# Optimization experiments

Hardware: AMD Instinct MI355X
Metric: run time of the kernel (lower is better)

Reference implementation:

```python
import jax, jax.numpy as jnp
import numpy as np

NEG_BIG = -9e15
ALPHA = 0.2  # leaky relu slope


def setup_inputs() -> dict:
    key = jax.random.key(0)
    k_h, k_adj, k_W, k_a = jax.random.split(key, 4)
    N, F_in, F_out = 8192, 512, 64
    h = jax.random.normal(k_h, (N, F_in), dtype=jnp.float32)
    adj = jax.random.randint(k_adj, (N, N), 0, 2, dtype=jnp.int32)
    adj = adj.at[jnp.arange(N), jnp.arange(N)].set(1)  # self-loops (add_self_loops)
    # xavier_uniform with gain=1.414
    limW = 1.414 * np.sqrt(6.0 / (F_in + F_out))
    W = jax.random.uniform(k_W, (F_in, F_out), jnp.float32, -limW, limW)
    lima = 1.414 * np.sqrt(6.0 / (2 * F_out + 1))
    a = jax.random.uniform(k_a, (2 * F_out, 1), jnp.float32, -lima, lima)
    return {"h": h, "adj": adj, "W": W, "a": a}


def reference(h, adj, W, a):
    F_out = W.shape[1]
    Wh = h @ W                                  # [N, F_out]
    # a_input[i,j] = concat(Wh[i], Wh[j]); a_input @ a == Wh@a1 + (Wh@a2)^T
    a1, a2 = a[:F_out, 0], a[F_out:, 0]
    src = Wh @ a1                               # [N]
    dst = Wh @ a2                               # [N]
    e = jax.nn.leaky_relu(src[:, None] + dst[None, :], ALPHA)  # [N, N]
    att = jnp.where(adj > 0, e, NEG_BIG)
    att = jax.nn.softmax(att, axis=1)
    # dropout is identity in eval mode (training=False)
    return att @ Wh                             # [N, F_out]
```

## Files before the change

kernel.cpp:

```cpp
#include <hip/hip_runtime.h>
#include <hip/hip_bf16.h>

#define N 8192
#define FIN 512
#define FOUT 64
#define L2E 1.44269504089f
#define SPLIT 8
#define MSTRIDE 34

typedef __attribute__((address_space(1))) const void* gas_cptr;
typedef __attribute__((address_space(3))) void* las_ptr;
typedef float f32x4 __attribute__((ext_vector_type(4)));
typedef short bf16x8 __attribute__((ext_vector_type(8)));

#if __has_builtin(__builtin_amdgcn_exp2f)
#define EXP2(x) __builtin_amdgcn_exp2f(x)
#else
#define EXP2(x) exp2f(x)
#endif

static __device__ __forceinline__ unsigned short f2bf_rne(float f) {
  unsigned u = __float_as_uint(f);
  u += 0x7FFFu + ((u >> 16) & 1u);
  return (unsigned short)(u >> 16);
}
static __device__ __forceinline__ unsigned fkey(float f) {
  unsigned u = __float_as_uint(f);
  return (u & 0x80000000u) ? ~u : (u | 0x80000000u);
}

__global__ __launch_bounds__(256) void k_wh(
    const float* __restrict__ h, const float* __restrict__ W,
    const float* __restrict__ a, unsigned short* __restrict__ WhT,
    float* __restrict__ src2, float* __restrict__ dst2,
    unsigned* __restrict__ dmaxk) {
  __shared__ __attribute__((aligned(16))) char wts[64 * 512 * 2];
  __shared__ __attribute__((aligned(16))) char hsb[2][64 * 64 * 2];

  const int t = threadIdx.x;
  const int w = t >> 6;
  const int ll = t & 63;
  const int lc = ll & 15;
  const int row0 = blockIdx.x * 64;

  {
    const int k0 = t * 2;
#pragma unroll
    for (int f4 = 0; f4 < 16; ++f4) {
      float4 x0 = *reinterpret_cast<const float4*>(&W[(size_t)k0 * FOUT + f4 * 4]);
      float4 x1 = *reinterpret_cast<const float4*>(&W[(size_t)(k0 + 1) * FOUT + f4 * 4]);
      const float e0[4] = {x0.x, x0.y, x0.z, x0.w};
      const float e1[4] = {x1.x, x1.y, x1.z, x1.w};
#pragma unroll
      for (int e = 0; e < 4; ++e) {
        int f = f4 * 4 + e;
        int bb = f * 1024 + k0 * 2;
        bb ^= (f & 7) << 4;
        *reinterpret_cast<ushort2*>(wts + bb) =
            make_ushort2(f2bf_rne(e0[e]), f2bf_rne(e1[e]));
      }
    }
  }
  __syncthreads();

  f32x4 acc[4];
#pragma unroll
  for (int c = 0; c < 4; ++c) acc[c] = (f32x4){0.f, 0.f, 0.f, 0.f};

  const int hrow = 16 * w + (ll >> 2);
  const float* hbase = &h[(size_t)(row0 + hrow) * FIN + (ll & 3) * 16];

#define LOADH(dst, kc)                                                        \
  do {                                                                        \
    dst[0] = *reinterpret_cast<const float4*>(hbase + (kc));                  \
    dst[1] = *reinterpret_cast<const float4*>(hbase + (kc) + 4);              \
    dst[2] = *reinterpret_cast<const float4*>(hbase + (kc) + 8);              \
    dst[3] = *reinterpret_cast<const float4*>(hbase + (kc) + 12);             \
  } while (0)

#define WRITEH(buf, src)                                                      \
  do {                                                                        \
    int bb0 = hrow * 128 + (ll & 3) * 32;                                     \
    bb0 ^= (hrow & 7) << 4;                                                   \
    _Pragma("unroll") for (int q = 0; q < 4; ++q) {                           \
      ushort4 u = make_ushort4(f2bf_rne(src[q].x), f2bf_rne(src[q].y),        \
                               f2bf_rne(src[q].z), f2bf_rne(src[q].w));       \
      *reinterpret_cast<ushort4*>(hsb[buf] + (bb0 ^ (q * 8))) = u;            \
    }                                                                         \
  } while (0)

#define MFMA_CHUNK(buf, kcb)                                                  \
  do {                                                                        \
    _Pragma("unroll") for (int k0 = 0; k0 < 2; ++k0) {                        \
      int arow = 16 * w + lc;                                                 \
      int ab = arow * 128 + k0 * 64 + ((ll >> 4) << 4);                       \
      ab ^= (arow & 7) << 4;                                                  \
      bf16x8 af = *reinterpret_cast<const bf16x8*>(hsb[buf] + ab);            \
      _Pragma("unroll") for (int c = 0; c < 4; ++c) {                         \
        int f = c * 16 + lc;                                                  \
        int bb = f * 1024 + (kcb) + k0 * 64 + ((ll >> 4) << 4);               \
        bb ^= (f & 7) << 4;                                                   \
        bf16x8 bfr = *reinterpret_cast<const bf16x8*>(wts + bb);              \
        acc[c] = __builtin_amdgcn_mfma_f32_16x16x32_bf16(af, bfr, acc[c], 0, 0, 0); \
      }                                                                       \
    }                                                                         \
  } while (0)

  float4 ha[4], hb[4];
  LOADH(ha, 0);
#pragma unroll
  for (int c2 = 0; c2 < 4; ++c2) {
    WRITEH(0, ha);
    LOADH(hb, (2 * c2 + 1) * 64);
    MFMA_CHUNK(0, (2 * c2) * 128);
    WRITEH(1, hb);
    if (c2 < 3) LOADH(ha, (2 * c2 + 2) * 64);
    MFMA_CHUNK(1, (2 * c2 + 1) * 128);
  }

  float a1v[4], a2v[4];
#pragma unroll
  for (int c = 0; c < 4; ++c) {
    a1v[c] = a[c * 16 + lc];
    a2v[c] = a[FOUT + c * 16 + lc];
  }
  float p1[4], p2[4];
#pragma unroll
  for (int q = 0; q < 4; ++q) {
    p1[q] = acc[0][q] * a1v[0] + acc[1][q] * a1v[1] + acc[2][q] * a1v[2] + acc[3][q] * a1v[3];
    p2[q] = acc[0][q] * a2v[0] + acc[1][q] * a2v[1] + acc[2][q] * a2v[2] + acc[3][q] * a2v[3];
  }
#pragma unroll
  for (int msk = 8; msk >= 1; msk >>= 1)
#pragma unroll
    for (int q = 0; q < 4; ++q) {
      p1[q] += __shfl_xor(p1[q], msk);
      p2[q] += __shfl_xor(p2[q], msk);
    }
#pragma unroll
  for (int q = 0; q < 4; ++q) { p1[q] *= L2E; p2[q] *= L2E; }

  const int r0 = row0 + 16 * w + ((ll >> 4) << 2);
  if (lc == 0) {
#pragma unroll
    for (int q = 0; q < 4; ++q) { src2[r0 + q] = p1[q]; dst2[r0 + q] = p2[q]; }
  }
#pragma unroll
  for (int c = 0; c < 4; ++c) {
    ushort4 u = make_ushort4(f2bf_rne(acc[c][0]), f2bf_rne(acc[c][1]),
                             f2bf_rne(acc[c][2]), f2bf_rne(acc[c][3]));
    *reinterpret_cast<ushort4*>(&WhT[(size_t)(c * 16 + lc) * N + r0]) = u;
  }
  float wm = fmaxf(fmaxf(p2[0], p2[1]), fmaxf(p2[2], p2[3]));
  wm = fmaxf(wm, __shfl_xor(wm, 16));
  wm = fmaxf(wm, __shfl_xor(wm, 32));
  if (ll == 0) atomicMax(dmaxk, fkey(wm));
#undef LOADH
#undef WRITEH
#undef MFMA_CHUNK
}

__global__ __launch_bounds__(256) void k_attn(
    const int* __restrict__ adj, const unsigned short* __restrict__ WhT,
    const float* __restrict__ src2, const float* __restrict__ dst2,
    const unsigned* __restrict__ dmaxk, float* __restrict__ out,
    float* __restrict__ Opart, float* __restrict__ lpart, const int split) {
  __shared__ unsigned mskd[64 * MSTRIDE];
  __shared__ __attribute__((aligned(16))) char pbs[8192];

  const int t = threadIdx.x;
  const int w = t >> 6;
  const int ll = t & 63;
  const int rg = t >> 4;
  const int cg = t & 15;
  const int i0 = rg * 4;
  const int lc = ll & 15;
  const int g16 = (ll >> 4) << 4;
  const int g8 = (ll >> 4) << 3;
  const int row0 = blockIdx.x * 64;
  const int jlen = N / split;
  const int jbase = blockIdx.y * jlen;

  unsigned kk = dmaxk[0];
  const float dmax2 = (kk & 0x80000000u) ? __uint_as_float(kk & 0x7FFFFFFFu)
                                         : __uint_as_float(~kk);

  float s2v[4], m2[4], l[4];
#pragma unroll
  for (int r = 0; r < 4; ++r) {
    s2v[r] = src2[row0 + i0 + r];
    float x = s2v[r] + dmax2;
    m2[r] = fmaxf(x, 0.2f * x);
    l[r] = 0.f;
  }

  f32x4 acc[4];
#pragma unroll
  for (int c = 0; c < 4; ++c) acc[c] = (f32x4){0.f, 0.f, 0.f, 0.f};

  const int bsh = (cg & 7) * 4;

  for (int mt = 0; mt < jlen; mt += 1024) {
    const int mbase = jbase + mt;

#pragma unroll 1
    for (int s = 0; s < 16; ++s) {
      const int row = 16 * w + s;
      const int* ar = adj + (size_t)(row0 + row) * N + mbase;
      unsigned x[16];
#pragma unroll
      for (int k = 0; k < 16; ++k) x[k] = ar[k * 64 + ll];
      unsigned long long b[16];
#pragma unroll
      for (int k = 0; k < 16; ++k) b[k] = __ballot(x[k] != 0);
      if (ll == 0) {
        unsigned long long* mrow =
            reinterpret_cast<unsigned long long*>(&mskd[row * MSTRIDE]);
#pragma unroll
        for (int k = 0; k < 16; ++k) mrow[k] = b[k];
      }
    }
    __syncthreads();

    unsigned mw[4], nmw[4];
    float dv[4], ndv[4];
#pragma unroll
    for (int r = 0; r < 4; ++r)
      mw[r] = mskd[(i0 + r) * MSTRIDE + (cg >> 3)];
    {
      float4 d_ = *reinterpret_cast<const float4*>(&dst2[mbase + cg * 4]);
      dv[0] = d_.x; dv[1] = d_.y; dv[2] = d_.z; dv[3] = d_.w;
    }

#pragma unroll 1
    for (int jt2 = 0; jt2 < 16; ++jt2) {
      const int j0 = mbase + jt2 * 64;

      bf16x8 bfr[2][4];
#pragma unroll
      for (int k0 = 0; k0 < 2; ++k0)
#pragma unroll
        for (int c = 0; c < 4; ++c)
          bfr[k0][c] = *reinterpret_cast<const bf16x8*>(
              &WhT[(size_t)(c * 16 + lc) * N + j0 + k0 * 32 + g8]);

      if (jt2 + 1 < 16) {
#pragma unroll
        for (int r = 0; r < 4; ++r)
          nmw[r] = mskd[(i0 + r) * MSTRIDE + (jt2 + 1) * 2 + (cg >> 3)];
        float4 d_ = *reinterpret_cast<const float4*>(&dst2[j0 + 64 + cg * 4]);
        ndv[0] = d_.x; ndv[1] = d_.y; ndv[2] = d_.z; ndv[3] = d_.w;
      }

      float p[4][4];
#pragma unroll
      for (int r = 0; r < 4; ++r) {
        unsigned b = mw[r] >> bsh;
#pragma unroll
        for (int jj = 0; jj < 4; ++jj) {
          float x = s2v[r] + dv[jj];
          float e2 = fmaxf(x, 0.2f * x);
          float pe = EXP2(e2 - m2[r]);
          pe = (b & (1u << jj)) ? pe : 0.f;
          p[r][jj] = pe;
          l[r] += pe;
        }
      }
#pragma unroll
      for (int r = 0; r < 4; ++r) {
        unsigned u0 = __float_as_uint(p[r][0]);
        unsigned u1 = __float_as_uint(p[r][1]);
        unsigned u2 = __float_as_uint(p[r][2]);
        unsigned u3 = __float_as_uint(p[r][3]);
        uint2 pk = make_uint2((u0 >> 16) | (u1 & 0xFFFF0000u),
                              (u2 >> 16) | (u3 & 0xFFFF0000u));
        int row = i0 + r;
        int ba = (row << 7) + (cg << 3);
        ba ^= (row & 7) << 4;
        *reinterpret_cast<uint2*>(pbs + ba) = pk;
      }

#pragma unroll
      for (int k0 = 0; k0 < 2; ++k0) {
        int arow = 16 * w + lc;
        int ab = (arow << 7) + k0 * 64 + g16;
        ab ^= (arow & 7) << 4;
        bf16x8 af = *reinterpret_cast<const bf16x8*>(pbs + ab);
#pragma unroll
        for (int c = 0; c < 4; ++c)
          acc[c] = __builtin_amdgcn_mfma_f32_16x16x32_bf16(af, bfr[k0][c],
                                                           acc[c], 0, 0, 0);
      }

      if (jt2 + 1 < 16) {
#pragma unroll
        for (int r = 0; r < 4; ++r) { mw[r] = nmw[r]; dv[r] = ndv[r]; }
      }
    }

    if (mt + 1024 < jlen) __syncthreads();
  }

#pragma unroll
  for (int msk = 8; msk >= 1; msk >>= 1)
#pragma unroll
    for (int r = 0; r < 4; ++r) l[r] += __shfl_xor(l[r], msk);

  const int orow = row0 + 16 * w + ((ll >> 4) << 2);
  const int ocol = ll & 15;
  if (split == 1) {
#pragma unroll
    for (int c = 0; c < 4; ++c)
#pragma unroll
      for (int q = 0; q < 4; ++q)
        out[(size_t)(orow + q) * FOUT + c * 16 + ocol] = acc[c][q] / l[q];
  } else {
    const int pb = blockIdx.y;
#pragma unroll
    for (int c = 0; c < 4; ++c)
#pragma unroll
      for (int q = 0; q < 4; ++q)
        Opart[((size_t)pb * N + orow + q) * FOUT + c * 16 + ocol] = acc[c][q];
    if (cg == 0) {
#pragma unroll
      for (int r = 0; r < 4; ++r)
        lpart[(size_t)pb * N + row0 + i0 + r] = l[r];
    }
  }
}

__global__ __launch_bounds__(256) void k_combine(
    const float* __restrict__ Opart, const float* __restrict__ lpart,
    float* __restrict__ out, const int split) {
  int idx = blockIdx.x * 256 + threadIdx.x;
  int row = idx >> 6;
  float num = 0.f, den = 0.f;
  for (int k = 0; k < split; ++k) {
    num += Opart[(size_t)k * N * FOUT + idx];
    den += lpart[(size_t)k * N + row];
  }
  out[idx] = num / den;
}

extern "C" void kernel_launch(void* const* d_in, const int* in_sizes, int n_in,
                              void* d_out, int out_size, void* d_ws, size_t ws_size,
                              hipStream_t stream) {
  const float* h = (const float*)d_in[0];
  const int* adj = (const int*)d_in[1];
  const float* W = (const float*)d_in[2];
  const float* a = (const float*)d_in[3];
  float* out = (float*)d_out;

  unsigned short* WhT = (unsigned short*)d_ws;
  float* src2 = (float*)(WhT + (size_t)FOUT * N);
  float* dst2 = src2 + N;
  unsigned* dmaxk = (unsigned*)(dst2 + N);
  float* Opart = (float*)(dmaxk + 64);

  const size_t base_bytes = (size_t)FOUT * N * 2 + 2 * N * 4 + 256;
  int split = SPLIT;
  while (split > 1 &&
         base_bytes + (size_t)split * ((size_t)N * FOUT + N) * 4 > ws_size)
    split >>= 1;
  float* lpart = Opart + (size_t)split * N * FOUT;

  hipMemsetAsync(dmaxk, 0, 4, stream);
  k_wh<<<dim3(N / 64), 256, 0, stream>>>(h, W, a, WhT, src2, dst2, dmaxk);
  k_attn<<<dim3(N / 64, split), 256, 0, stream>>>(adj, WhT, src2, dst2, dmaxk,
                                                  out, Opart, lpart, split);
  if (split > 1)
    k_combine<<<dim3((N * FOUT) / 256), 256, 0, stream>>>(Opart, lpart, out, split);
}
```

Measured before the change: 130.6 us.

## Read adjacency directly per thread with register prefetch instead of LDS bitmask staging

The attention kernel no longer stages the adjacency tile into a shared-memory bitmask via ballots and barriers. Each thread now loads its own int4 adjacency slices and dst values straight from global memory, with a four-deep register prefetch ring. This removes the per-1024-column barrier and the ballot staging step. The split is fixed at compile time, which drops the workspace-size fallback and assumes the workspace is always large enough. Register pressure rises, and the A-fragment load now contains redundant overwritten loads.

```diff
diff --git a/kernel.cpp b/kernel.cpp
--- a/kernel.cpp
+++ b/kernel.cpp
@@ -6,7 +6,7 @@
 #define FOUT 64
 #define L2E 1.44269504089f
 #define SPLIT 8
-#define MSTRIDE 34
+#define NTILES ((N / SPLIT) / 64)
 
 typedef __attribute__((address_space(1))) const void* gas_cptr;
 typedef __attribute__((address_space(3))) void* las_ptr;
@@ -164,8 +164,7 @@
     const int* __restrict__ adj, const unsigned short* __restrict__ WhT,
     const float* __restrict__ src2, const float* __restrict__ dst2,
     const unsigned* __restrict__ dmaxk, float* __restrict__ out,
-    float* __restrict__ Opart, float* __restrict__ lpart, const int split) {
-  __shared__ unsigned mskd[64 * MSTRIDE];
+    float* __restrict__ Opart, float* __restrict__ lpart) {
   __shared__ __attribute__((aligned(16))) char pbs[8192];
 
   const int t = threadIdx.x;
@@ -178,8 +177,7 @@
   const int g16 = (ll >> 4) << 4;
   const int g8 = (ll >> 4) << 3;
   const int row0 = blockIdx.x * 64;
-  const int jlen = N / split;
-  const int jbase = blockIdx.y * jlen;
+  const int jbase = blockIdx.y * (N / SPLIT);
 
   unsigned kk = dmaxk[0];
   const float dmax2 = (kk & 0x80000000u) ? __uint_as_float(kk & 0x7FFFFFFFu)
@@ -198,43 +196,40 @@
 #pragma unroll
   for (int c = 0; c < 4; ++c) acc[c] = (f32x4){0.f, 0.f, 0.f, 0.f};
 
-  const int bsh = (cg & 7) * 4;
-
-  for (int mt = 0; mt < jlen; mt += 1024) {
-    const int mbase = jbase + mt;
-
-#pragma unroll 1
-    for (int s = 0; s < 16; ++s) {
-      const int row = 16 * w + s;
-      const int* ar = adj + (size_t)(row0 + row) * N + mbase;
-      unsigned x[16];
-#pragma unroll
-      for (int k = 0; k < 16; ++k) x[k] = ar[k * 64 + ll];
-      unsigned long long b[16];
-#pragma unroll
-      for (int k = 0; k < 16; ++k) b[k] = __ballot(x[k] != 0);
-      if (ll == 0) {
-        unsigned long long* mrow =
-            reinterpret_cast<unsigned long long*>(&mskd[row * MSTRIDE]);
-#pragma unroll
-        for (int k = 0; k < 16; ++k) mrow[k] = b[k];
-      }
-    }
-    __syncthreads();
-
-    unsigned mw[4], nmw[4];
-    float dv[4], ndv[4];
-#pragma unroll
-    for (int r = 0; r < 4; ++r)
-      mw[r] = mskd[(i0 + r) * MSTRIDE + (cg >> 3)];
-    {
-      float4 d_ = *reinterpret_cast<const float4*>(&dst2[mbase + cg * 4]);
-      dv[0] = d_.x; dv[1] = d_.y; dv[2] = d_.z; dv[3] = d_.w;
-    }
-
-#pragma unroll 1
-    for (int jt2 = 0; jt2 < 16; ++jt2) {
-      const int j0 = mbase + jt2 * 64;
+  const int bsh = 0;
+  (void)bsh;
+
+  const int* ar0 = adj + (size_t)(row0 + i0 + 0) * N + jbase + cg * 4;
+  const int* ar1 = adj + (size_t)(row0 + i0 + 1) * N + jbase + cg * 4;
+  const int* ar2 = adj + (size_t)(row0 + i0 + 2) * N + jbase + cg * 4;
+  const int* ar3 = adj + (size_t)(row0 + i0 + 3) * N + jbase + cg * 4;
+  const float* dp = dst2 + jbase + cg * 4;
+
+  int4 aS[4][4];
+  float4 dS[4];
+
+#define LOADT(s, jt_)                                                         \
+  do {                                                                        \
+    const int o_ = (jt_) * 64;                                                \
+    aS[s][0] = *reinterpret_cast<const int4*>(ar0 + o_);                      \
+    aS[s][1] = *reinterpret_cast<const int4*>(ar1 + o_);                      \
+    aS[s][2] = *reinterpret_cast<const int4*>(ar2 + o_);                      \
+    aS[s][3] = *reinterpret_cast<const int4*>(ar3 + o_);                      \
+    dS[s] = *reinterpret_cast<const float4*>(dp + o_);                        \
+  } while (0)
+
+#pragma unroll
+  for (int s = 0; s < 4; ++s) LOADT(s, s);
+
+  const int arow = 16 * w + lc;
+  int abz = (arow << 7);
+  abz ^= (arow & 7) << 4;
+
+  for (int jt4 = 0; jt4 < NTILES / 4; ++jt4) {
+#pragma unroll
+    for (int i = 0; i < 4; ++i) {
+      const int jt = jt4 * 4 + i;
+      const int j0 = jbase + jt * 64;
 
       bf16x8 bfr[2][4];
 #pragma unroll
@@ -244,28 +239,24 @@
           bfr[k0][c] = *reinterpret_cast<const bf16x8*>(
               &WhT[(size_t)(c * 16 + lc) * N + j0 + k0 * 32 + g8]);
 
-      if (jt2 + 1 < 16) {
-#pragma unroll
-        for (int r = 0; r < 4; ++r)
-          nmw[r] = mskd[(i0 + r) * MSTRIDE + (jt2 + 1) * 2 + (cg >> 3)];
-        float4 d_ = *reinterpret_cast<const float4*>(&dst2[j0 + 64 + cg * 4]);
-        ndv[0] = d_.x; ndv[1] = d_.y; ndv[2] = d_.z; ndv[3] = d_.w;
-      }
-
       float p[4][4];
 #pragma unroll
       for (int r = 0; r < 4; ++r) {
-        unsigned b = mw[r] >> bsh;
+        const int aw[4] = {aS[i][r].x, aS[i][r].y, aS[i][r].z, aS[i][r].w};
+        const float dvv[4] = {dS[i].x, dS[i].y, dS[i].z, dS[i].w};
 #pragma unroll
         for (int jj = 0; jj < 4; ++jj) {
-          float x = s2v[r] + dv[jj];
+          float x = s2v[r] + dvv[jj];
           float e2 = fmaxf(x, 0.2f * x);
           float pe = EXP2(e2 - m2[r]);
-          pe = (b & (1u << jj)) ? pe : 0.f;
+          pe = aw[jj] > 0 ? pe : 0.f;
           p[r][jj] = pe;
           l[r] += pe;
         }
       }
+
+      if (jt4 < NTILES / 4 - 1) LOADT(i, jt + 4);
+
 #pragma unroll
       for (int r = 0; r < 4; ++r) {
         unsigned u0 = __float_as_uint(p[r][0]);
@@ -282,24 +273,21 @@
 
 #pragma unroll
       for (int k0 = 0; k0 < 2; ++k0) {
-        int arow = 16 * w + lc;
-        int ab = (arow << 7) + k0 * 64 + g16;
-        ab ^= (arow & 7) << 4;
-        bf16x8 af = *reinterpret_cast<const bf16x8*>(pbs + ab);
+        bf16x8 af = *reinterpret_cast<const bf16x8*>(pbs + (abz ^ (k0 * 64)) + k0 * 64 + g16 - (abz & 0) );
+        af = *reinterpret_cast<const bf16x8*>(pbs + ((abz + k0 * 64 + g16) ^ 0));
+        {
+          int ab = (arow << 7) + k0 * 64 + g16;
+          ab ^= (arow & 7) << 4;
+          af = *reinterpret_cast<const bf16x8*>(pbs + ab);
+        }
 #pragma unroll
         for (int c = 0; c < 4; ++c)
           acc[c] = __builtin_amdgcn_mfma_f32_16x16x32_bf16(af, bfr[k0][c],
                                                            acc[c], 0, 0, 0);
       }
-
-      if (jt2 + 1 < 16) {
-#pragma unroll
-        for (int r = 0; r < 4; ++r) { mw[r] = nmw[r]; dv[r] = ndv[r]; }
-      }
     }
-
-    if (mt + 1024 < jlen) __syncthreads();
-  }
+  }
+#undef LOADT
 
 #pragma unroll
   for (int msk = 8; msk >= 1; msk >>= 1)
@@ -308,34 +296,27 @@
 
   const int orow = row0 + 16 * w + ((ll >> 4) << 2);
   const int ocol = ll & 15;
-  if (split == 1) {
-#pragma unroll
-    for (int c = 0; c < 4; ++c)
-#pragma unroll
-      for (int q = 0; q < 4; ++q)
-        out[(size_t)(orow + q) * FOUT + c * 16 + ocol] = acc[c][q] / l[q];
-  } else {
-    const int pb = blockIdx.y;
-#pragma unroll
-    for (int c = 0; c < 4; ++c)
-#pragma unroll
-      for (int q = 0; q < 4; ++q)
-        Opart[((size_t)pb * N + orow + q) * FOUT + c * 16 + ocol] = acc[c][q];
-    if (cg == 0) {
-#pragma unroll
-      for (int r = 0; r < 4; ++r)
-        lpart[(size_t)pb * N + row0 + i0 + r] = l[r];
-    }
+  const int pb = blockIdx.y;
+#pragma unroll
+  for (int c = 0; c < 4; ++c)
+#pragma unroll
+    for (int q = 0; q < 4; ++q)
+      Opart[((size_t)pb * N + orow + q) * FOUT + c * 16 + ocol] = acc[c][q];
+  if (cg == 0) {
+#pragma unroll
+    for (int r = 0; r < 4; ++r)
+      lpart[(size_t)pb * N + row0 + i0 + r] = l[r];
   }
 }
 
 __global__ __launch_bounds__(256) void k_combine(
     const float* __restrict__ Opart, const float* __restrict__ lpart,
-    float* __restrict__ out, const int split) {
+    float* __restrict__ out) {
   int idx = blockIdx.x * 256 + threadIdx.x;
   int row = idx >> 6;
   float num = 0.f, den = 0.f;
-  for (int k = 0; k < split; ++k) {
+#pragma unroll
+  for (int k = 0; k < SPLIT; ++k) {
     num += Opart[(size_t)k * N * FOUT + idx];
     den += lpart[(size_t)k * N + row];
   }
@@ -356,18 +337,11 @@
   float* dst2 = src2 + N;
   unsigned* dmaxk = (unsigned*)(dst2 + N);
   float* Opart = (float*)(dmaxk + 64);
-
-  const size_t base_bytes = (size_t)FOUT * N * 2 + 2 * N * 4 + 256;
-  int split = SPLIT;
-  while (split > 1 &&
-         base_bytes + (size_t)split * ((size_t)N * FOUT + N) * 4 > ws_size)
-    split >>= 1;
-  float* lpart = Opart + (size_t)split * N * FOUT;
+  float* lpart = Opart + (size_t)SPLIT * N * FOUT;
 
   hipMemsetAsync(dmaxk, 0, 4, stream);
   k_wh<<<dim3(N / 64), 256, 0, stream>>>(h, W, a, WhT, src2, dst2, dmaxk);
-  k_attn<<<dim3(N / 64, split), 256, 0, stream>>>(adj, WhT, src2, dst2, dmaxk,
-                                                  out, Opart, lpart, split);
-  if (split > 1)
-    k_combine<<<dim3((N * FOUT) / 256), 256, 0, stream>>>(Opart, lpart, out, split);
-}
+  k_attn<<<dim3(N / 64, SPLIT), 256, 0, stream>>>(adj, WhT, src2, dst2, dmaxk,
+                                                  out, Opart, lpart);
+  k_combine<<<dim3((N * FOUT) / 256), 256, 0, stream>>>(Opart, lpart, out);
+}
```

Result: faster. 126.0 us (-3.5%).
